# Kernel tuning notes

Hardware: AMD Instinct MI355X
Metric: run time of the kernel (lower is better)

Reference implementation:

```python
import jax, jax.numpy as jnp
import numpy as np

B, S, D = 8, 2048, 1024  # batch, seq_len, emb_dim == qkv_dim
NEG = -999999.0  # module uses -999999 instead of -inf


def setup_inputs() -> dict:
    key = jax.random.key(0)
    ks = jax.random.split(key, 4)
    inputs = jax.random.normal(ks[0], (B, S, D), dtype=jnp.float32)
    # causal mask, flax attention layout [B, 1, S, S]
    causal = jnp.tril(jnp.ones((S, S), dtype=bool))
    mask = jnp.broadcast_to(causal, (B, 1, S, S))
    scale = 1.0 / np.sqrt(D)
    Wq = jax.random.normal(ks[1], (D, D), dtype=jnp.float32) * scale
    Wk = jax.random.normal(ks[2], (D, D), dtype=jnp.float32) * scale
    Wv = jax.random.normal(ks[3], (D, D), dtype=jnp.float32) * scale
    z = jnp.zeros((D,), dtype=jnp.float32)
    return {"inputs": inputs, "mask": mask, "Wq": Wq, "bq": z, "Wk": Wk,
            "bk": z, "Wv": Wv, "bv": z}


def reference(inputs, mask, Wq, bq, Wk, bk, Wv, bv):
    q = inputs @ Wq + bq  # [B,S,D]
    k = inputs @ Wk + bk
    v = inputs @ Wv + bv
    depth = q.shape[-1]
    q = q / jnp.sqrt(jnp.asarray(depth, q.dtype))
    attn = jnp.einsum('bqd,bkd->bqk', q, k)  # [B,S,S]
    attn = jnp.where(jnp.squeeze(mask, axis=1), attn, NEG)
    attn = jax.nn.softmax(attn, axis=-1)
    return attn @ v  # [B,S,D]
```

## Files before the change

kernel.cpp:

```cpp
#include <hip/hip_runtime.h>
#include <hip/hip_bf16.h>
#include <cstdint>

#define S_LEN 2048
#define D_DIM 1024
#define NB 8

typedef __attribute__((ext_vector_type(8))) short bf16x8;
typedef __attribute__((ext_vector_type(4))) float f32x4;

__device__ __forceinline__ unsigned short f2bf(float f) {
  union { float f; unsigned u; } x; x.f = f;
  unsigned r = x.u + 0x7fffu + ((x.u >> 16) & 1u);
  return (unsigned short)(r >> 16);
}
__device__ __forceinline__ float bf2f(unsigned short b) {
  union { unsigned u; float f; } x; x.u = ((unsigned)b) << 16;
  return x.f;
}
__device__ __forceinline__ void gload16(const void* g, void* l) {
  __builtin_amdgcn_global_load_lds((const __attribute__((address_space(1))) void*)g,
                                   (__attribute__((address_space(3))) void*)l, 16, 0, 0);
}

__global__ __launch_bounds__(256)
void prep(const float* __restrict__ X, const float* __restrict__ W0,
          const float* __restrict__ W1, const float* __restrict__ W2,
          unsigned short* __restrict__ Xb, unsigned short* __restrict__ Wt) {
  __shared__ unsigned short tile[32][33];
  int bid = blockIdx.x, tid = threadIdx.x;
  if (bid < 16384) {
    int i = bid * 256 + tid;
    float4 v = reinterpret_cast<const float4*>(X)[i];
    ushort4 o;
    o.x = f2bf(v.x); o.y = f2bf(v.y); o.z = f2bf(v.z); o.w = f2bf(v.w);
    reinterpret_cast<ushort4*>(Xb)[i] = o;
    return;
  }
  int f = bid - 16384;
  int zc = f >> 10, rem = f & 1023, by = (rem >> 5) * 32, bx = (rem & 31) * 32;
  const float* in = (zc == 0) ? W0 : (zc == 1 ? W1 : W2);
  unsigned short* o = Wt + (size_t)zc * 1048576;
  int tx = tid & 31, ty = tid >> 5;
  #pragma unroll
  for (int i = ty; i < 32; i += 8)
    tile[i][tx] = f2bf(in[(size_t)(by + i) * D_DIM + bx + tx]);
  __syncthreads();
  #pragma unroll
  for (int i = ty; i < 32; i += 8)
    o[(size_t)(bx + i) * D_DIM + by + tx] = tile[tx][i];
}

__global__ __launch_bounds__(256)
void combine_pv(float* __restrict__ O, const unsigned short* __restrict__ part,
                const float* __restrict__ rs) {
  int i = blockIdx.x * 256 + threadIdx.x;
  if (i >= 2097152) return;
  int e = i * 4;
  int z = e >> 20;
  int rem = e & 1048575;
  int r = rem >> 10;
  int col = rem & 1023;
  float inv = 1.f / rs[z * S_LEN + 1024 + r];
  float4 o = *reinterpret_cast<const float4*>(&O[(size_t)z * S_LEN * D_DIM + (size_t)(1024 + r) * 1024 + col]);
  ushort4 p = *reinterpret_cast<const ushort4*>(&part[((size_t)z * 1024 + r) * 1024 + col]);
  o.x = (o.x + bf2f(p.x)) * inv;
  o.y = (o.y + bf2f(p.y)) * inv;
  o.z = (o.z + bf2f(p.z)) * inv;
  o.w = (o.w + bf2f(p.w)) * inv;
  *reinterpret_cast<float4*>(&O[(size_t)z * S_LEN * D_DIM + (size_t)(1024 + r) * 1024 + col]) = o;
}

template<int MODE>
__global__ __launch_bounds__(512, 2)
void gemm8(const unsigned short* __restrict__ Aall, const unsigned short* __restrict__ Btall,
           void* __restrict__ Call, int Kd, int lda, int ldb, int ldc,
           long sAz, long sBz, long sCz,
           const float* __restrict__ b0, const float* __restrict__ b1,
           const float* __restrict__ b2, float* __restrict__ rowsum,
           unsigned short* __restrict__ part, int ntn) {
  __shared__ __align__(16) unsigned short As[4][8192];
  __shared__ __align__(16) unsigned short Bs[4][8192];
  int bid = blockIdx.x;
  int t = threadIdx.x, lane = t & 63, w = t >> 6;

  if (MODE == 1 && bid >= 288) {
    int v = bid - 288;
    int z = v >> 5, c0 = (v & 31) * 32;
    const unsigned short* V = Aall + (size_t)z * sAz + 2048;
    unsigned short* out = part + (size_t)z * (1024L * 2048) + (size_t)c0 * 2048;
    unsigned short* tl = &As[0][0];
    int tx = t & 31, ty = t >> 5;
    int i2 = t & 63, j0 = t >> 6;
    for (int r0 = 0; r0 < S_LEN; r0 += 64) {
      #pragma unroll
      for (int ii = ty; ii < 64; ii += 16)
        tl[ii * 33 + tx] = V[(size_t)(r0 + ii) * 3072 + c0 + tx];
      __syncthreads();
      #pragma unroll
      for (int jj = j0; jj < 32; jj += 8)
        out[(size_t)jj * 2048 + r0 + i2] = tl[i2 * 33 + jj];
      __syncthreads();
    }
    return;
  }

  int nwg = (MODE == 1) ? 288 : gridDim.x;
  int wg = (bid & 7) * (nwg >> 3) + (bid >> 3);
  int z, tm, tn, kt0, nkt, m2c = 0;
  if (MODE == 0) {
    z = 0; tm = wg / ntn; tn = wg % ntn; kt0 = 0; nkt = Kd >> 5;
  } else if (MODE == 1) {
    z = wg / 36; int f = wg % 36;
    tm = 0;
    while ((tm + 1) * (tm + 2) / 2 <= f) ++tm;
    tn = f - tm * (tm + 1) / 2;
    kt0 = 0; nkt = Kd >> 5;
  } else {
    z = wg / 48; int r = wg % 48; tn = r / 12; int f = r % 12;
    const int tmT[12] = {0,1,2,3,4,4,5,5,6,6,7,7};
    const int cT[12]  = {0,0,0,0,0,1,0,1,0,1,0,1};
    tm = tmT[f]; int c = cT[f];
    int kts = (tm + 1) * 8;
    if (tm < 4) { kt0 = 0; nkt = kts; m2c = 0; }
    else { int half = kts >> 1; kt0 = c ? half : 0; nkt = c ? (kts - half) : half; m2c = 1 + c; }
  }
  const unsigned short* A  = Aall  + (size_t)z * sAz;
  const unsigned short* Bt = Btall + (size_t)z * sBz;
  int m0 = tm * 256, n0 = tn * 256;
  int wr = w >> 2, wc = w & 3;
  int lr = lane & 15, lq = lane >> 4;
  long triBase = (long)(tm * (tm + 1) / 2) * 65536;

  int offA[8], offB[4];
  #pragma unroll
  for (int mi = 0; mi < 8; ++mi) {
    int row = wr * 128 + mi * 16 + lr;
    offA[mi] = row * 32 + ((lq ^ ((row >> 1) & 3)) * 8);
  }
  #pragma unroll
  for (int ni = 0; ni < 4; ++ni) {
    int row = wc * 64 + ni * 16 + lr;
    offB[ni] = row * 32 + ((lq ^ ((row >> 1) & 3)) * 8);
  }
  int srow[2], soff[2];
  #pragma unroll
  for (int c = 0; c < 2; ++c) {
    int r = c * 128 + w * 16 + (lane >> 2);
    srow[c] = r;
    soff[c] = ((lane & 3) ^ ((r >> 1) & 3)) * 8;
  }

  f32x4 acc[8][4];
  f32x4 zero4 = {0.f, 0.f, 0.f, 0.f};
  #pragma unroll
  for (int mi = 0; mi < 8; ++mi)
    #pragma unroll
    for (int ni = 0; ni < 4; ++ni) acc[mi][ni] = zero4;

  auto stgA = [&](int buf, int kg) {
    #pragma unroll
    for (int c = 0; c < 2; ++c) {
      const unsigned short* src;
      if (MODE == 2)
        src = A + triBase + (long)(kg >> 3) * 65536 + srow[c] * 256 + (kg & 7) * 32 + soff[c];
      else
        src = A + (size_t)(m0 + srow[c]) * lda + kg * 32 + soff[c];
      gload16(src, &As[buf][c * 4096 + w * 512]);
    }
  };
  auto stgB = [&](int buf, int kg) {
    #pragma unroll
    for (int c = 0; c < 2; ++c)
      gload16(Bt + (size_t)(n0 + srow[c]) * ldb + kg * 32 + soff[c],
              &Bs[buf][c * 4096 + w * 512]);
  };

  stgA(0, kt0); stgB(0, kt0); stgA(1, kt0 + 1); stgB(1, kt0 + 1);
  asm volatile("s_waitcnt vmcnt(4)" ::: "memory");
  __builtin_amdgcn_s_barrier();

  for (int i = 0; i < nkt; ++i) {
    const int bcur = i & 3, bpre = (i + 2) & 3;
    const bool stg = (i + 2 < nkt);
    const int kg = kt0 + i;
    const unsigned short* Ac = As[bcur];
    const unsigned short* Bc = Bs[bcur];
    bf16x8 af[4], bfv[4];

    #pragma unroll
    for (int q = 0; q < 4; ++q) af[q]  = *reinterpret_cast<const bf16x8*>(&Ac[offA[q]]);
    #pragma unroll
    for (int q = 0; q < 4; ++q) bfv[q] = *reinterpret_cast<const bf16x8*>(&Bc[offB[q]]);
    if (stg) stgA(bpre, kg + 2);
    __builtin_amdgcn_s_barrier();
    asm volatile("s_waitcnt lgkmcnt(0)" ::: "memory");
    __builtin_amdgcn_sched_barrier(0);
    __builtin_amdgcn_s_setprio(1);
    #pragma unroll
    for (int q = 0; q < 4; ++q)
      #pragma unroll
      for (int j = 0; j < 4; ++j)
        acc[q][j] = __builtin_amdgcn_mfma_f32_16x16x32_bf16(af[q], bfv[j], acc[q][j], 0, 0, 0);
    __builtin_amdgcn_s_setprio(0);
    __builtin_amdgcn_s_barrier();

    #pragma unroll
    for (int q = 0; q < 4; ++q) af[q] = *reinterpret_cast<const bf16x8*>(&Ac[offA[4 + q]]);
    if (stg) stgB(bpre, kg + 2);
    if (i + 2 < nkt)      asm volatile("s_waitcnt vmcnt(4)" ::: "memory");
    else if (i + 1 < nkt) asm volatile("s_waitcnt vmcnt(0)" ::: "memory");
    __builtin_amdgcn_s_barrier();
    asm volatile("s_waitcnt lgkmcnt(0)" ::: "memory");
    __builtin_amdgcn_sched_barrier(0);
    __builtin_amdgcn_s_setprio(1);
    #pragma unroll
    for (int q = 0; q < 4; ++q)
      #pragma unroll
      for (int j = 0; j < 4; ++j)
        acc[4 + q][j] = __builtin_amdgcn_mfma_f32_16x16x32_bf16(af[q], bfv[j], acc[4 + q][j], 0, 0, 0);
    __builtin_amdgcn_s_setprio(0);
    __builtin_amdgcn_s_barrier();
  }
  __syncthreads();

  unsigned short* ep = &As[0][0] + w * 4096;
  int lq4 = lq << 4;

  if (MODE == 0) {
    unsigned short* C = (unsigned short*)Call;
    #pragma unroll
    for (int mh = 0; mh < 2; ++mh) {
      #pragma unroll
      for (int mi2 = 0; mi2 < 4; ++mi2)
        #pragma unroll
        for (int ni = 0; ni < 4; ++ni) {
          int col = ni * 16 + lr;
          int gcol = n0 + wc * 64 + col;
          float bb, sc;
          if (gcol < 1024)      { bb = b0[gcol];        sc = 0.03125f; }
          else if (gcol < 2048) { bb = b1[gcol - 1024]; sc = 1.0f; }
          else                  { bb = b2[gcol - 2048]; sc = 1.0f; }
          #pragma unroll
          for (int j = 0; j < 4; ++j) {
            int lrow = mi2 * 16 + lq * 4 + j;
            ep[lrow * 64 + (col ^ lq4)] = f2bf((acc[mh * 4 + mi2][ni][j] + bb) * sc);
          }
        }
      asm volatile("s_waitcnt lgkmcnt(0)" ::: "memory");
      #pragma unroll
      for (int pass = 0; pass < 8; ++pass) {
        int rrow = pass * 8 + (lane >> 3);
        int c8 = (lane & 7) * 8;
        int sw = ((rrow >> 2) & 3) << 4;
        bf16x8 vv = *reinterpret_cast<const bf16x8*>(&ep[rrow * 64 + (c8 ^ sw)]);
        int grow = m0 + wr * 128 + mh * 64 + rrow;
        *reinterpret_cast<bf16x8*>(&C[(size_t)grow * ldc + n0 + wc * 64 + c8]) = vv;
      }
      asm volatile("s_waitcnt lgkmcnt(0)" ::: "memory");
    }
  } else if (MODE == 1) {
    unsigned short* Ct = (unsigned short*)Call + (size_t)z * sCz + triBase + (long)tn * 65536;
    float* rs = rowsum + z * S_LEN;
    #pragma unroll
    for (int mh = 0; mh < 2; ++mh) {
      #pragma unroll
      for (int mi2 = 0; mi2 < 4; ++mi2)
        #pragma unroll
        for (int j = 0; j < 4; ++j) {
          int lrow = mi2 * 16 + lq * 4 + j;
          int grow = m0 + wr * 128 + mh * 64 + lrow;
          float partial = 0.f;
          #pragma unroll
          for (int ni = 0; ni < 4; ++ni) {
            int col = ni * 16 + lr;
            int gcol = n0 + wc * 64 + col;
            float e = (gcol <= grow) ? __expf(acc[mh * 4 + mi2][ni][j]) : 0.f;
            partial += e;
            ep[lrow * 64 + (col ^ lq4)] = f2bf(e);
          }
          #pragma unroll
          for (int off = 1; off < 16; off <<= 1) partial += __shfl_xor(partial, off);
          if (lr == 0) atomicAdd(&rs[grow], partial);
        }
      asm volatile("s_waitcnt lgkmcnt(0)" ::: "memory");
      #pragma unroll
      for (int pass = 0; pass < 8; ++pass) {
        int rrow = pass * 8 + (lane >> 3);
        int c8 = (lane & 7) * 8;
        int sw = ((rrow >> 2) & 3) << 4;
        bf16x8 vv = *reinterpret_cast<const bf16x8*>(&ep[rrow * 64 + (c8 ^ sw)]);
        int lrow2 = wr * 128 + mh * 64 + rrow;
        *reinterpret_cast<bf16x8*>(&Ct[(size_t)lrow2 * 256 + wc * 64 + c8]) = vv;
      }
      asm volatile("s_waitcnt lgkmcnt(0)" ::: "memory");
    }
  } else {
    float* C = (float*)Call + (size_t)z * sCz;
    const float* rs = rowsum + z * S_LEN;
    #pragma unroll
    for (int mi = 0; mi < 8; ++mi)
      #pragma unroll
      for (int j = 0; j < 4; ++j) {
        int row = m0 + wr * 128 + mi * 16 + lq * 4 + j;
        if (m2c == 0) {
          float inv = 1.f / rs[row];
          #pragma unroll
          for (int ni = 0; ni < 4; ++ni) {
            int col = n0 + wc * 64 + ni * 16 + lr;
            C[(size_t)row * ldc + col] = acc[mi][ni][j] * inv;
          }
        } else if (m2c == 1) {
          #pragma unroll
          for (int ni = 0; ni < 4; ++ni) {
            int col = n0 + wc * 64 + ni * 16 + lr;
            C[(size_t)row * ldc + col] = acc[mi][ni][j];
          }
        } else {
          unsigned short* P = part + ((size_t)z * 1024 + (row - 1024)) * 1024;
          #pragma unroll
          for (int ni = 0; ni < 4; ++ni) {
            int col = n0 + wc * 64 + ni * 16 + lr;
            P[col] = f2bf(acc[mi][ni][j]);
          }
        }
      }
  }
}

extern "C" void kernel_launch(void* const* d_in, const int* in_sizes, int n_in,
                              void* d_out, int out_size, void* d_ws, size_t ws_size,
                              hipStream_t stream) {
  (void)in_sizes; (void)n_in; (void)out_size; (void)ws_size;
  const float* X  = (const float*)d_in[0];
  const float* Wq = (const float*)d_in[2];
  const float* bq = (const float*)d_in[3];
  const float* Wk = (const float*)d_in[4];
  const float* bk = (const float*)d_in[5];
  const float* Wv = (const float*)d_in[6];
  const float* bv = (const float*)d_in[7];

  char* ws = (char*)d_ws;
  unsigned short* Xb  = (unsigned short*)(ws);
  unsigned short* Wt  = (unsigned short*)(ws + 33554432L);
  float*          Rs  = (float*)(ws + 33554432L);
  unsigned short* QKV = (unsigned short*)(ws + 39845888L);
  unsigned short* Pb  = (unsigned short*)(ws + 140509184L);
  unsigned short* Prt = (unsigned short*)(ws + 178257920L);
  unsigned short* Vt  = Xb;

  prep<<<19456, 256, 0, stream>>>(X, Wq, Wk, Wv, Xb, Wt);
  gemm8<0><<<dim3(64 * 12, 1, 1), 512, 0, stream>>>(Xb, Wt, (void*)QKV,
      D_DIM, D_DIM, D_DIM, 3 * D_DIM,
      0L, 0L, 0L, bq, bk, bv, nullptr, nullptr, 12);
  hipMemsetAsync(Rs, 0, NB * S_LEN * sizeof(float), stream);
  gemm8<1><<<dim3(288 + 256, 1, 1), 512, 0, stream>>>(QKV, QKV + 1024, (void*)Pb,
      D_DIM, 3 * D_DIM, 3 * D_DIM, 256,
      (long)S_LEN * 3 * D_DIM, (long)S_LEN * 3 * D_DIM, 36L * 65536L,
      nullptr, nullptr, nullptr, Rs, Vt, 0);
  gemm8<2><<<dim3(384, 1, 1), 512, 0, stream>>>(Pb, Vt, d_out,
      S_LEN, 0, S_LEN, D_DIM,
      36L * 65536L, (long)D_DIM * S_LEN, (long)S_LEN * D_DIM,
      nullptr, nullptr, nullptr, Rs, Prt, 0);
  combine_pv<<<8192, 256, 0, stream>>>((float*)d_out, Prt, Rs);
}
```

Baseline: 319.4 us.

## Replace split-K partial buffer and combine kernel with atomic adds into output

For the split-K tiles of the PV GEMM, both halves now scale by the row-sum reciprocal and atomically add fp32 results into the output, instead of writing a bf16 partial buffer that a separate combine kernel merged. The zeroing of the lower half of the output and of the row-sum buffer moves into the prep kernel, removing the memset and the combine launch. Row sums get their own workspace region so they no longer alias Wt. This trades an extra kernel and bf16 round-trip traffic for fp32 atomics on half the output rows, with a nondeterministic summation order.

New measurement: 334.9 us. +4.9%, slower.

```diff
diff --git a/kernel.cpp b/kernel.cpp
--- a/kernel.cpp
+++ b/kernel.cpp
@@ -26,7 +26,8 @@
 __global__ __launch_bounds__(256)
 void prep(const float* __restrict__ X, const float* __restrict__ W0,
           const float* __restrict__ W1, const float* __restrict__ W2,
-          unsigned short* __restrict__ Xb, unsigned short* __restrict__ Wt) {
+          unsigned short* __restrict__ Xb, unsigned short* __restrict__ Wt,
+          float* __restrict__ Od, float* __restrict__ Rs) {
   __shared__ unsigned short tile[32][33];
   int bid = blockIdx.x, tid = threadIdx.x;
   if (bid < 16384) {
@@ -37,38 +38,30 @@
     reinterpret_cast<ushort4*>(Xb)[i] = o;
     return;
   }
-  int f = bid - 16384;
-  int zc = f >> 10, rem = f & 1023, by = (rem >> 5) * 32, bx = (rem & 31) * 32;
-  const float* in = (zc == 0) ? W0 : (zc == 1 ? W1 : W2);
-  unsigned short* o = Wt + (size_t)zc * 1048576;
-  int tx = tid & 31, ty = tid >> 5;
-  #pragma unroll
-  for (int i = ty; i < 32; i += 8)
-    tile[i][tx] = f2bf(in[(size_t)(by + i) * D_DIM + bx + tx]);
-  __syncthreads();
-  #pragma unroll
-  for (int i = ty; i < 32; i += 8)
-    o[(size_t)(bx + i) * D_DIM + by + tx] = tile[tx][i];
-}
-
-__global__ __launch_bounds__(256)
-void combine_pv(float* __restrict__ O, const unsigned short* __restrict__ part,
-                const float* __restrict__ rs) {
-  int i = blockIdx.x * 256 + threadIdx.x;
-  if (i >= 2097152) return;
-  int e = i * 4;
-  int z = e >> 20;
-  int rem = e & 1048575;
-  int r = rem >> 10;
-  int col = rem & 1023;
-  float inv = 1.f / rs[z * S_LEN + 1024 + r];
-  float4 o = *reinterpret_cast<const float4*>(&O[(size_t)z * S_LEN * D_DIM + (size_t)(1024 + r) * 1024 + col]);
-  ushort4 p = *reinterpret_cast<const ushort4*>(&part[((size_t)z * 1024 + r) * 1024 + col]);
-  o.x = (o.x + bf2f(p.x)) * inv;
-  o.y = (o.y + bf2f(p.y)) * inv;
-  o.z = (o.z + bf2f(p.z)) * inv;
-  o.w = (o.w + bf2f(p.w)) * inv;
-  *reinterpret_cast<float4*>(&O[(size_t)z * S_LEN * D_DIM + (size_t)(1024 + r) * 1024 + col]) = o;
+  if (bid < 19456) {
+    int f = bid - 16384;
+    int zc = f >> 10, rem = f & 1023, by = (rem >> 5) * 32, bx = (rem & 31) * 32;
+    const float* in = (zc == 0) ? W0 : (zc == 1 ? W1 : W2);
+    unsigned short* o = Wt + (size_t)zc * 1048576;
+    int tx = tid & 31, ty = tid >> 5;
+    #pragma unroll
+    for (int i = ty; i < 32; i += 8)
+      tile[i][tx] = f2bf(in[(size_t)(by + i) * D_DIM + bx + tx]);
+    __syncthreads();
+    #pragma unroll
+    for (int i = ty; i < 32; i += 8)
+      o[(size_t)(bx + i) * D_DIM + by + tx] = tile[tx][i];
+    return;
+  }
+  float4 z4 = {0.f, 0.f, 0.f, 0.f};
+  if (bid < 27648) {
+    int i = (bid - 19456) * 256 + tid;
+    int z = i >> 18, rem = i & 262143;
+    reinterpret_cast<float4*>(Od)[(size_t)z * 524288 + 262144 + rem] = z4;
+    return;
+  }
+  int i = (bid - 27648) * 256 + tid;
+  reinterpret_cast<float4*>(Rs)[i] = z4;
 }
 
 template<int MODE>
@@ -123,7 +116,7 @@
     tm = tmT[f]; int c = cT[f];
     int kts = (tm + 1) * 8;
     if (tm < 4) { kt0 = 0; nkt = kts; m2c = 0; }
-    else { int half = kts >> 1; kt0 = c ? half : 0; nkt = c ? (kts - half) : half; m2c = 1 + c; }
+    else { int half = kts >> 1; kt0 = c ? half : 0; nkt = c ? (kts - half) : half; m2c = 1; }
   }
   const unsigned short* A  = Aall  + (size_t)z * sAz;
   const unsigned short* Bt = Btall + (size_t)z * sBz;
@@ -303,25 +296,18 @@
       #pragma unroll
       for (int j = 0; j < 4; ++j) {
         int row = m0 + wr * 128 + mi * 16 + lq * 4 + j;
+        float inv = 1.f / rs[row];
         if (m2c == 0) {
-          float inv = 1.f / rs[row];
           #pragma unroll
           for (int ni = 0; ni < 4; ++ni) {
             int col = n0 + wc * 64 + ni * 16 + lr;
             C[(size_t)row * ldc + col] = acc[mi][ni][j] * inv;
           }
-        } else if (m2c == 1) {
+        } else {
           #pragma unroll
           for (int ni = 0; ni < 4; ++ni) {
             int col = n0 + wc * 64 + ni * 16 + lr;
-            C[(size_t)row * ldc + col] = acc[mi][ni][j];
-          }
-        } else {
-          unsigned short* P = part + ((size_t)z * 1024 + (row - 1024)) * 1024;
-          #pragma unroll
-          for (int ni = 0; ni < 4; ++ni) {
-            int col = n0 + wc * 64 + ni * 16 + lr;
-            P[col] = f2bf(acc[mi][ni][j]);
+            atomicAdd(&C[(size_t)row * ldc + col], acc[mi][ni][j] * inv);
           }
         }
       }
@@ -343,17 +329,15 @@
   char* ws = (char*)d_ws;
   unsigned short* Xb  = (unsigned short*)(ws);
   unsigned short* Wt  = (unsigned short*)(ws + 33554432L);
-  float*          Rs  = (float*)(ws + 33554432L);
   unsigned short* QKV = (unsigned short*)(ws + 39845888L);
   unsigned short* Pb  = (unsigned short*)(ws + 140509184L);
-  unsigned short* Prt = (unsigned short*)(ws + 178257920L);
+  float*          Rs  = (float*)(ws + 178257920L);
   unsigned short* Vt  = Xb;
 
-  prep<<<19456, 256, 0, stream>>>(X, Wq, Wk, Wv, Xb, Wt);
+  prep<<<27664, 256, 0, stream>>>(X, Wq, Wk, Wv, Xb, Wt, (float*)d_out, Rs);
   gemm8<0><<<dim3(64 * 12, 1, 1), 512, 0, stream>>>(Xb, Wt, (void*)QKV,
       D_DIM, D_DIM, D_DIM, 3 * D_DIM,
       0L, 0L, 0L, bq, bk, bv, nullptr, nullptr, 12);
-  hipMemsetAsync(Rs, 0, NB * S_LEN * sizeof(float), stream);
   gemm8<1><<<dim3(288 + 256, 1, 1), 512, 0, stream>>>(QKV, QKV + 1024, (void*)Pb,
       D_DIM, 3 * D_DIM, 3 * D_DIM, 256,
       (long)S_LEN * 3 * D_DIM, (long)S_LEN * 3 * D_DIM, 36L * 65536L,
@@ -361,6 +345,5 @@
   gemm8<2><<<dim3(384, 1, 1), 512, 0, stream>>>(Pb, Vt, d_out,
       S_LEN, 0, S_LEN, D_DIM,
       36L * 65536L, (long)D_DIM * S_LEN, (long)S_LEN * D_DIM,
-      nullptr, nullptr, nullptr, Rs, Prt, 0);
-  combine_pv<<<8192, 256, 0, stream>>>((float*)d_out, Prt, Rs);
-}
+      nullptr, nullptr, nullptr, Rs, nullptr, 0);
+}
```
